# Kernel tuning notes

Hardware: AMD Instinct MI355X
Metric: run time of the kernel (lower is better)

The kernel has to match this reference:

```python
import jax, jax.numpy as jnp
import numpy as np

B, T, D, H, O = 2048, 512, 24, 100, 2


def setup_inputs() -> dict:
    key = jax.random.key(0)
    ks = jax.random.split(key, 8)
    init = lambda k, shape, fan: (jax.random.normal(k, shape, jnp.float32) / np.sqrt(fan).astype(np.float32))
    return {
        "input_seq": jax.random.normal(ks[0], (B, T, D), jnp.float32),
        "ts": jax.random.uniform(ks[1], (B, T), jnp.float32),
        # TimeLSTM params (stored transposed vs torch.nn.Linear: [in, out])
        "W_all": init(ks[2], (H, 4 * H), H),   # recurrent -> 4 gates
        "b_all": jnp.zeros((4 * H,), jnp.float32),
        "U_all": init(ks[3], (D, 4 * H), D),   # input -> 4 gates
        "b_u": jnp.zeros((4 * H,), jnp.float32),
        "W_d": init(ks[4], (H, H), H),         # time-decay on cell
        "b_d": jnp.zeros((H,), jnp.float32),
        # output head
        "W_lin": init(ks[5], (H, O), H),
        "b_lin": jnp.zeros((O,), jnp.float32),
    }


def _time_lstm_last(input_seq, ts, W_all, b_all, U_all, b_u, W_d, b_d):
    """Time-aware LSTM scan; returns final hidden state [B, H]."""
    b, t, d = input_seq.shape
    h_dim = W_d.shape[0]
    # Precompute input projections for all steps once: [T, B, 4H]
    u = jnp.einsum('btd,dk->tbk', input_seq, U_all) + b_u
    ts_t = jnp.swapaxes(ts, 0, 1)[..., None]  # [T, B, 1]

    def step(carry, xs):
        h, c = carry
        u_t, t_t = xs
        # time-aware cell decomposition
        c_s1 = jnp.tanh(c @ W_d + b_d)              # short-term component
        c_adj = (c - c_s1) + c_s1 * t_t             # long-term + decayed short-term
        gates = jax.nn.sigmoid(h @ W_all + b_all + u_t)  # [B, 4H]
        f, i, o, c_tmp = jnp.split(gates, 4, axis=1)     # chunk order: f, i, o, c~
        c_new = f * c_adj + i * c_tmp
        h_new = o * jnp.tanh(c_new)
        return (h_new, c_new), None

    z = jnp.zeros((b, h_dim), input_seq.dtype)
    (h_last, _), _ = jax.lax.scan(step, (z, z), (u, ts_t))
    return h_last


def reference(input_seq, ts, W_all, b_all, U_all, b_u, W_d, b_d, W_lin, b_lin):
    # seq_lstm.forward: TimeLSTM -> take last timestep -> Linear -> ReLU
    h_last = _time_lstm_last(input_seq, ts, W_all, b_all, U_all, b_u, W_d, b_d)
    return jax.nn.relu(h_last @ W_lin + b_lin)  # [B, O]
```

## Files before the change

kernel.cpp:

```cpp
#include <hip/hip_runtime.h>
#include <hip/hip_bf16.h>


typedef __attribute__((ext_vector_type(8))) short bf16x8;
typedef __attribute__((ext_vector_type(4))) float f32x4;

#define B_SZ 2048
#define T_SZ 512
#define D_SZ 24
#define H_SZ 100
#define O_SZ 2

__device__ __forceinline__ unsigned short f2bf(float v) {
    return __builtin_bit_cast(unsigned short, __float2bfloat16(v));
}
__device__ __forceinline__ float fexp2(float x) { return __builtin_amdgcn_exp2f(x); }
__device__ __forceinline__ float frcp (float x) { return __builtin_amdgcn_rcpf(x); }
__device__ __forceinline__ float sigm(float x) { return frcp(1.0f + fexp2(-1.44269504f * x)); }
__device__ __forceinline__ float tanh_(float x) {
    return __builtin_fmaf(-2.0f, frcp(1.0f + fexp2(2.88539008f * x)), 1.0f);
}

__global__ __launch_bounds__(512, 2) void tlstm_kernel(
    const float* __restrict__ input_seq, const float* __restrict__ ts,
    const float* __restrict__ W_all, const float* __restrict__ b_all,
    const float* __restrict__ U_all, const float* __restrict__ b_u,
    const float* __restrict__ W_d,  const float* __restrict__ b_d,
    const float* __restrict__ W_lin, const float* __restrict__ b_lin,
    float* __restrict__ out)
{
    __shared__ unsigned short hx[2][16 * 128];
    __shared__ unsigned short cx[2][16 * 128];
    __shared__ float ts_lds[2][8];
    __shared__ float hl[8][H_SZ];

    const int tid   = (int)threadIdx.x;
    const int lane  = tid & 63;
    const int wave  = tid >> 6;
    const int row16 = lane & 15;
    const int kgrp  = lane >> 4;
    const int rowbase = (int)blockIdx.x * 8;

    for (int i = tid; i < 2 * 16 * 128; i += 512) {
        const int p = i >> 11, r = (i >> 7) & 15, k = i & 127;
        const unsigned short v = (r < 8 && k == 124) ? (unsigned short)0x3F80 : (unsigned short)0;
        const int idx = r * 128 + (k ^ ((r & 7) << 3));
        hx[p][idx] = v;
        cx[p][idx] = v;
    }

    const int jj = wave * 16 + row16;
    bf16x8 Bf[5][4];
    #pragma unroll
    for (int t = 0; t < 5; ++t) {
        #pragma unroll
        for (int g = 0; g < 4; ++g) {
            bf16x8 fr;
            #pragma unroll
            for (int e = 0; e < 8; ++e) {
                const int k = g * 32 + kgrp * 8 + e;
                float v = 0.0f;
                if (jj < H_SZ) {
                    if (t < 4) {
                        const int n = t * H_SZ + jj;
                        if (k < 100)       v = W_all[k * 400 + n];
                        else if (k < 124)  v = U_all[(k - 100) * 400 + n];
                        else if (k == 124) v = b_all[n] + b_u[n];
                    } else {
                        if (k < 100)       v = W_d[k * 100 + jj];
                        else if (k == 124) v = b_d[jj];
                    }
                }
                fr[e] = (short)f2bf(v);
            }
            Bf[t][g] = fr;
        }
    }

    __syncthreads();

    if (wave == 7) {
        #pragma unroll
        for (int q = 0; q < 3; ++q) {
            const int ii = lane * 3 + q;
            const int r = ii / 24, d = ii % 24;
            const float v = input_seq[((size_t)(rowbase + r) * T_SZ + 0) * D_SZ + d];
            hx[0][r * 128 + ((100 + d) ^ ((r & 7) << 3))] = f2bf(v);
        }
        if (lane < 8) ts_lds[0][lane] = ts[(size_t)(rowbase + lane) * T_SZ + 0];
    }

    const bool hi  = (lane >= 32);
    const int  rb2 = (((lane & 31) >> 4) << 2) + (hi ? 2 : 0);
    const bool epi = (wave < 7) && (jj < H_SZ);
    float cst[2] = {0.f, 0.f};

    __syncthreads();

    int par = 0;
    for (int s = 0; s < T_SZ; ++s) {
        const unsigned short* hp = hx[par];
        const unsigned short* cp = cx[par];

        if (wave < 7) {
            bf16x8 ah[4], ac[4];
            #pragma unroll
            for (int g = 0; g < 4; ++g) {
                const int idx = row16 * 128 + ((g * 32 + kgrp * 8) ^ ((row16 & 7) << 3));
                ah[g] = *(const bf16x8*)(hp + idx);
                ac[g] = *(const bf16x8*)(cp + idx);
            }

            f32x4 acc[5];
            #pragma unroll
            for (int t = 0; t < 4; ++t) {
                f32x4 a = {0.f, 0.f, 0.f, 0.f};
                #pragma unroll
                for (int g = 0; g < 4; ++g)
                    a = __builtin_amdgcn_mfma_f32_16x16x32_bf16(ah[g], Bf[t][g], a, 0, 0, 0);
                acc[t] = a;
            }
            {
                f32x4 a = {0.f, 0.f, 0.f, 0.f};
                #pragma unroll
                for (int g = 0; g < 4; ++g)
                    a = __builtin_amdgcn_mfma_f32_16x16x32_bf16(ac[g], Bf[4][g], a, 0, 0, 0);
                acc[4] = a;
            }

            float p[2][5];
            #pragma unroll
            for (int t = 0; t < 5; ++t) {
                const float s2 = __shfl_xor(acc[t][2], 32, 64);
                const float s3 = __shfl_xor(acc[t][3], 32, 64);
                p[0][t] = hi ? s2 : acc[t][0];
                p[1][t] = hi ? s3 : acc[t][1];
            }

            if (epi) {
                unsigned short* hn = hx[par ^ 1];
                unsigned short* cn = cx[par ^ 1];
                #pragma unroll
                for (int e = 0; e < 2; ++e) {
                    const int r = rb2 + e;
                    const float tsv = ts_lds[par][r];
                    const float f = sigm(p[e][0]);
                    const float i = sigm(p[e][1]);
                    const float o = sigm(p[e][2]);
                    const float g = sigm(p[e][3]);
                    const float cs = tanh_(p[e][4]);
                    const float ca = cst[e] + cs * (tsv - 1.0f);
                    cst[e] = f * ca + i * g;
                    const float h = o * tanh_(cst[e]);
                    const int ix = r * 128 + (jj ^ ((r & 7) << 3));
                    hn[ix] = f2bf(h);
                    cn[ix] = f2bf(cst[e]);
                    if (s == T_SZ - 1) hl[r][jj] = h;
                }
            }
        } else {
            const int s1 = (s + 1 < T_SZ) ? (s + 1) : s;
            #pragma unroll
            for (int q = 0; q < 3; ++q) {
                const int ii = lane * 3 + q;
                const int r = ii / 24, d = ii % 24;
                const float v = input_seq[((size_t)(rowbase + r) * T_SZ + s1) * D_SZ + d];
                hx[par ^ 1][r * 128 + ((100 + d) ^ ((r & 7) << 3))] = f2bf(v);
            }
            if (lane < 8) ts_lds[par ^ 1][lane] = ts[(size_t)(rowbase + lane) * T_SZ + s1];
        }

        __syncthreads();
        par ^= 1;
    }

    {
        const int r  = tid >> 6;
        const int o  = (tid >> 5) & 1;
        const int k0 = tid & 31;
        float part = 0.f;
        for (int k = k0; k < H_SZ; k += 32)
            part += hl[r][k] * W_lin[k * O_SZ + o];
        #pragma unroll
        for (int off = 16; off; off >>= 1)
            part += __shfl_xor(part, off, 64);
        if (k0 == 0)
            out[(size_t)(rowbase + r) * O_SZ + o] = fmaxf(part + b_lin[o], 0.f);
    }
}

extern "C" void kernel_launch(void* const* d_in, const int* in_sizes, int n_in,
                              void* d_out, int out_size, void* d_ws, size_t ws_size,
                              hipStream_t stream) {
    const float* input_seq = (const float*)d_in[0];
    const float* ts_p      = (const float*)d_in[1];
    const float* W_all     = (const float*)d_in[2];
    const float* b_all     = (const float*)d_in[3];
    const float* U_all     = (const float*)d_in[4];
    const float* b_u       = (const float*)d_in[5];
    const float* W_d       = (const float*)d_in[6];
    const float* b_d       = (const float*)d_in[7];
    const float* W_lin     = (const float*)d_in[8];
    const float* b_lin     = (const float*)d_in[9];

    tlstm_kernel<<<dim3(B_SZ / 8), dim3(512), 0, stream>>>(
        input_seq, ts_p, W_all, b_all, U_all, b_u, W_d, b_d, W_lin, b_lin,
        (float*)d_out);
}
```

Baseline: 623.2 us.

## Pack h and c into one MFMA A tile with four rows per block

Each block now handles four batch rows instead of eight. The h state and the c state are written into the same 16-row LDS tile, in duplicated and permuted row slots, so one set of A-fragment loads serves both the gate MFMAs and the decay MFMA. The epilogue is reworked so each lane computes one row and one hidden unit, with fewer cross-lane shuffles. The grid doubles and launch bounds rise to four blocks per CU so more blocks run in parallel on the serial timestep chain. The cost is double the number of blocks, each running the same 512-step loop with its own barriers and redundant weight-fragment setup.

```diff
diff --git a/kernel.cpp b/kernel.cpp
--- a/kernel.cpp
+++ b/kernel.cpp
@@ -10,6 +10,7 @@
 #define D_SZ 24
 #define H_SZ 100
 #define O_SZ 2
+#define RPB 4
 
 __device__ __forceinline__ unsigned short f2bf(float v) {
     return __builtin_bit_cast(unsigned short, __float2bfloat16(v));
@@ -21,7 +22,7 @@
     return __builtin_fmaf(-2.0f, frcp(1.0f + fexp2(2.88539008f * x)), 1.0f);
 }
 
-__global__ __launch_bounds__(512, 2) void tlstm_kernel(
+__global__ __launch_bounds__(512, 4) void tlstm_kernel(
     const float* __restrict__ input_seq, const float* __restrict__ ts,
     const float* __restrict__ W_all, const float* __restrict__ b_all,
     const float* __restrict__ U_all, const float* __restrict__ b_u,
@@ -30,23 +31,21 @@
     float* __restrict__ out)
 {
     __shared__ unsigned short hx[2][16 * 128];
-    __shared__ unsigned short cx[2][16 * 128];
-    __shared__ float ts_lds[2][8];
-    __shared__ float hl[8][H_SZ];
+    __shared__ float ts_lds[2][RPB];
+    __shared__ float hl[RPB][H_SZ];
 
     const int tid   = (int)threadIdx.x;
     const int lane  = tid & 63;
     const int wave  = tid >> 6;
     const int row16 = lane & 15;
     const int kgrp  = lane >> 4;
-    const int rowbase = (int)blockIdx.x * 8;
+    const int G     = lane >> 4;
+    const int rowbase = (int)blockIdx.x * RPB;
 
     for (int i = tid; i < 2 * 16 * 128; i += 512) {
         const int p = i >> 11, r = (i >> 7) & 15, k = i & 127;
-        const unsigned short v = (r < 8 && k == 124) ? (unsigned short)0x3F80 : (unsigned short)0;
-        const int idx = r * 128 + (k ^ ((r & 7) << 3));
-        hx[p][idx] = v;
-        cx[p][idx] = v;
+        const unsigned short v = (k == 124) ? (unsigned short)0x3F80 : (unsigned short)0;
+        hx[p][r * 128 + (k ^ ((r & 7) << 3))] = v;
     }
 
     const int jj = wave * 16 + row16;
@@ -83,109 +82,110 @@
         #pragma unroll
         for (int q = 0; q < 3; ++q) {
             const int ii = lane * 3 + q;
-            const int r = ii / 24, d = ii % 24;
-            const float v = input_seq[((size_t)(rowbase + r) * T_SZ + 0) * D_SZ + d];
-            hx[0][r * 128 + ((100 + d) ^ ((r & 7) << 3))] = f2bf(v);
+            const int r8 = ii / 24, d = ii % 24;
+            const int tr = (r8 < 4) ? r8 : 8 + r8;
+            const float v = input_seq[((size_t)(rowbase + (r8 & 3)) * T_SZ + 0) * D_SZ + d];
+            hx[0][tr * 128 + ((100 + d) ^ ((tr & 7) << 3))] = f2bf(v);
         }
-        if (lane < 8) ts_lds[0][lane] = ts[(size_t)(rowbase + lane) * T_SZ + 0];
-    }
-
-    const bool hi  = (lane >= 32);
-    const int  rb2 = (((lane & 31) >> 4) << 2) + (hi ? 2 : 0);
+        if (lane < RPB) ts_lds[0][lane] = ts[(size_t)(rowbase + lane) * T_SZ + 0];
+    }
+
+    const int r = (G == 0) ? 0 : (G == 1) ? 2 : (G == 2) ? 1 : 3;
     const bool epi = (wave < 7) && (jj < H_SZ);
-    float cst[2] = {0.f, 0.f};
+    const int ixh0 = (r     ) * 128 + (jj ^ (((r     ) & 7) << 3));
+    const int ixh1 = (12 + r) * 128 + (jj ^ (((12 + r) & 7) << 3));
+    const int ixc0 = (4 + r ) * 128 + (jj ^ (((4 + r ) & 7) << 3));
+    const int ixc1 = (8 + r ) * 128 + (jj ^ (((8 + r ) & 7) << 3));
+    float cst = 0.f;
 
     __syncthreads();
 
     int par = 0;
     for (int s = 0; s < T_SZ; ++s) {
         const unsigned short* hp = hx[par];
-        const unsigned short* cp = cx[par];
 
         if (wave < 7) {
-            bf16x8 ah[4], ac[4];
+            bf16x8 a4[4];
             #pragma unroll
             for (int g = 0; g < 4; ++g) {
                 const int idx = row16 * 128 + ((g * 32 + kgrp * 8) ^ ((row16 & 7) << 3));
-                ah[g] = *(const bf16x8*)(hp + idx);
-                ac[g] = *(const bf16x8*)(cp + idx);
+                a4[g] = *(const bf16x8*)(hp + idx);
             }
 
             f32x4 acc[5];
             #pragma unroll
-            for (int t = 0; t < 4; ++t) {
+            for (int t = 0; t < 5; ++t) {
                 f32x4 a = {0.f, 0.f, 0.f, 0.f};
                 #pragma unroll
                 for (int g = 0; g < 4; ++g)
-                    a = __builtin_amdgcn_mfma_f32_16x16x32_bf16(ah[g], Bf[t][g], a, 0, 0, 0);
+                    a = __builtin_amdgcn_mfma_f32_16x16x32_bf16(a4[g], Bf[t][g], a, 0, 0, 0);
                 acc[t] = a;
             }
-            {
-                f32x4 a = {0.f, 0.f, 0.f, 0.f};
-                #pragma unroll
-                for (int g = 0; g < 4; ++g)
-                    a = __builtin_amdgcn_mfma_f32_16x16x32_bf16(ac[g], Bf[4][g], a, 0, 0, 0);
-                acc[4] = a;
-            }
-
-            float p[2][5];
-            #pragma unroll
-            for (int t = 0; t < 5; ++t) {
-                const float s2 = __shfl_xor(acc[t][2], 32, 64);
-                const float s3 = __shfl_xor(acc[t][3], 32, 64);
-                p[0][t] = hi ? s2 : acc[t][0];
-                p[1][t] = hi ? s3 : acc[t][1];
-            }
+
+            float swg1[4], swg2[4];
+            #pragma unroll
+            for (int t = 0; t < 4; ++t) {
+                swg1[t] = __shfl_xor(acc[t][1], 32, 64);
+                swg2[t] = __shfl_xor(acc[t][2], 32, 64);
+            }
+            const float swd0 = __shfl_xor(acc[4][0], 32, 64);
+            const float swd3 = __shfl_xor(acc[4][3], 32, 64);
 
             if (epi) {
                 unsigned short* hn = hx[par ^ 1];
-                unsigned short* cn = cx[par ^ 1];
+                float gg[4];
                 #pragma unroll
-                for (int e = 0; e < 2; ++e) {
-                    const int r = rb2 + e;
-                    const float tsv = ts_lds[par][r];
-                    const float f = sigm(p[e][0]);
-                    const float i = sigm(p[e][1]);
-                    const float o = sigm(p[e][2]);
-                    const float g = sigm(p[e][3]);
-                    const float cs = tanh_(p[e][4]);
-                    const float ca = cst[e] + cs * (tsv - 1.0f);
-                    cst[e] = f * ca + i * g;
-                    const float h = o * tanh_(cst[e]);
-                    const int ix = r * 128 + (jj ^ ((r & 7) << 3));
-                    hn[ix] = f2bf(h);
-                    cn[ix] = f2bf(cst[e]);
-                    if (s == T_SZ - 1) hl[r][jj] = h;
-                }
+                for (int t = 0; t < 4; ++t)
+                    gg[t] = (G == 0) ? acc[t][0] : (G == 1) ? swg2[t]
+                          : (G == 2) ? swg1[t]   : acc[t][3];
+                const float dd = (G == 0) ? swd0 : (G == 1) ? acc[4][2]
+                               : (G == 2) ? acc[4][1] : swd3;
+
+                const float tsv = ts_lds[par][r];
+                const float f = sigm(gg[0]);
+                const float i = sigm(gg[1]);
+                const float o = sigm(gg[2]);
+                const float g = sigm(gg[3]);
+                const float cs = tanh_(dd);
+                const float ca = cst + cs * (tsv - 1.0f);
+                cst = f * ca + i * g;
+                const float h = o * tanh_(cst);
+
+                const unsigned short hb = f2bf(h);
+                const unsigned short cb = f2bf(cst);
+                hn[ixh0] = hb;  hn[ixh1] = hb;
+                hn[ixc0] = cb;  hn[ixc1] = cb;
+                if (s == T_SZ - 1) hl[r][jj] = h;
             }
         } else {
             const int s1 = (s + 1 < T_SZ) ? (s + 1) : s;
             #pragma unroll
             for (int q = 0; q < 3; ++q) {
                 const int ii = lane * 3 + q;
-                const int r = ii / 24, d = ii % 24;
-                const float v = input_seq[((size_t)(rowbase + r) * T_SZ + s1) * D_SZ + d];
-                hx[par ^ 1][r * 128 + ((100 + d) ^ ((r & 7) << 3))] = f2bf(v);
-            }
-            if (lane < 8) ts_lds[par ^ 1][lane] = ts[(size_t)(rowbase + lane) * T_SZ + s1];
+                const int r8 = ii / 24, d = ii % 24;
+                const int tr = (r8 < 4) ? r8 : 8 + r8;
+                const float v = input_seq[((size_t)(rowbase + (r8 & 3)) * T_SZ + s1) * D_SZ + d];
+                hx[par ^ 1][tr * 128 + ((100 + d) ^ ((tr & 7) << 3))] = f2bf(v);
+            }
+            if (lane < RPB) ts_lds[par ^ 1][lane] = ts[(size_t)(rowbase + lane) * T_SZ + s1];
         }
 
         __syncthreads();
         par ^= 1;
     }
 
-    {
-        const int r  = tid >> 6;
+    if (tid < 64 * RPB) {
+        const int rr = tid >> 6;
         const int o  = (tid >> 5) & 1;
         const int k0 = tid & 31;
         float part = 0.f;
         for (int k = k0; k < H_SZ; k += 32)
-            part += hl[r][k] * W_lin[k * O_SZ + o];
+            part += hl[rr][k] * W_lin[k * O_SZ + o];
         #pragma unroll
         for (int off = 16; off; off >>= 1)
             part += __shfl_xor(part, off, 64);
         if (k0 == 0)
-            out[(size_t)(rowbase + r) * O_SZ + o] = fmaxf(part + b_lin[o], 0.f);
+            out[(size_t)(rowbase + rr) * O_SZ + o] = fmaxf(part + b_lin[o], 0.f);
     }
 }
 
@@ -203,7 +203,7 @@
     const float* W_lin     = (const float*)d_in[8];
     const float* b_lin     = (const float*)d_in[9];
 
-    tlstm_kernel<<<dim3(B_SZ / 8), dim3(512), 0, stream>>>(
+    tlstm_kernel<<<dim3(B_SZ / RPB), dim3(512), 0, stream>>>(
         input_seq, ts_p, W_all, b_all, U_all, b_u, W_d, b_d, W_lin, b_lin,
         (float*)d_out);
 }
```

Result: slower. 1.912 ms (+206.7%).
